# Performance work log

Measured on AMD Instinct MI355X. Metric: run time of the kernel, lower is better.

## Reference

```python
import jax, jax.numpy as jnp
import numpy as np

B, N, E = 64, 512, 8192          # graphs, nodes per graph, edges per graph
F_IN, H, C = 128, 128, 10        # in features, hidden, classes
K1, K2 = 256, 128                # dense pool cluster counts: ceil(.5*N), ceil(.5*K1)
EPS = 1e-15


def setup_inputs():
    key = jax.random.key(0)
    keys = jax.random.split(key, 32)
    it = iter(keys)
    def w(shape, fan_in):
        return jax.random.normal(next(it), shape, jnp.float32) / np.sqrt(fan_in)
    x = jax.random.normal(next(it), (B * N, F_IN), jnp.float32)
    src_l = jax.random.randint(next(it), (B, E), 0, N)
    dst_l = jax.random.randint(next(it), (B, E), 0, N)
    off = (jnp.arange(B) * N)[:, None]
    src = (src_l + off).reshape(-1).astype(jnp.int32)
    dst = (dst_l + off).reshape(-1).astype(jnp.int32)
    return dict(
        x=x, src=src, dst=dst,
        conv0_wr=w((F_IN, H), F_IN), conv0_wroot=w((F_IN, H), F_IN), conv0_b=jnp.zeros((H,), jnp.float32),
        sconv2_wr=w((H, H), H), sconv2_wroot=w((H, H), H), sconv2_b=jnp.zeros((H,), jnp.float32),
        sconv3_wr=w((H, H), H), sconv3_wroot=w((H, H), H), sconv3_b=jnp.zeros((H,), jnp.float32),
        sage1_wr=w((H, H), H), sage1_wroot=w((H, H), H), sage1_b=jnp.zeros((H,), jnp.float32),
        sage2_wr=w((H, H), H), sage2_wroot=w((H, H), H), sage2_b=jnp.zeros((H,), jnp.float32),
        pool0_w=w((H, K1), H), pool0_b=jnp.zeros((K1,), jnp.float32),
        pool1_w=w((H, K2), H), pool1_b=jnp.zeros((K2,), jnp.float32),
        p1=w((H,), H), p2=w((H,), H), p3=w((H,), H),
        lin1_1_w=w((2 * H, H), 2 * H), lin1_1_b=jnp.zeros((H,), jnp.float32),
        lin1_w=w((H, H), H), lin1_b=jnp.zeros((H,), jnp.float32),
        lin2_w=w((2 * H, C), 2 * H), lin2_b=jnp.zeros((C,), jnp.float32),
    )


def _graph_conv(x, src, dst, emask, wr, wroot, b, n):
    # PyG GraphConv: lin_rel(sum_j x_j) + lin_root(x_i); invalid edges masked to 0.
    msg = x[src] * emask[:, None]
    agg = jax.ops.segment_sum(msg, dst, num_segments=n)
    return agg @ wr + x @ wroot + b


def _topk_pool(x, score_w, src, dst, emask, n_per_graph, k):
    # TopK pooling (MPoolS): score = x.w/||w||, keep top ratio*n per graph, gate by tanh(score).
    score = x @ score_w / (jnp.linalg.norm(score_w) + 1e-16)
    idx = jax.lax.top_k(score.reshape(B, n_per_graph), k)[1]
    perm = (idx + (jnp.arange(B) * n_per_graph)[:, None]).reshape(-1)
    new_x = x[perm] * jnp.tanh(score[perm])[:, None]
    new_id = jnp.full((B * n_per_graph,), -1, jnp.int32).at[perm].set(
        jnp.arange(B * k, dtype=jnp.int32))
    ns, nd = new_id[src], new_id[dst]
    valid = (ns >= 0) & (nd >= 0) & (emask > 0)
    return new_x, jnp.where(valid, ns, 0), jnp.where(valid, nd, 0), valid.astype(x.dtype)


def _readout(x, k):
    # gmp || gap per graph (nodes are contiguous, k per graph)
    xr = x.reshape(B, k, -1)
    return jnp.concatenate([xr.max(axis=1), xr.mean(axis=1)], axis=-1)


def _dense_sage(x, adj, wr, wroot, b):
    agg = (adj @ x) / jnp.clip(adj.sum(-1, keepdims=True), 1.0, None)
    return agg @ wr + x @ wroot + b


def _dense_mincut_pool(x, adj, s):
    s = jax.nn.softmax(s, axis=-1)
    k = s.shape[-1]
    out = jnp.einsum('bnk,bnf->bkf', s, x)
    out_adj = jnp.einsum('bnk,bnm,bml->bkl', s, adj, s)
    mincut_num = jnp.trace(out_adj, axis1=-2, axis2=-1)
    deg = adj.sum(-1)
    mincut_den = jnp.einsum('bn,bnk,bnk->b', deg, s, s)
    mc = -jnp.mean(mincut_num / (mincut_den + EPS))
    ss = jnp.einsum('bnk,bnl->bkl', s, s)
    ss_n = jnp.linalg.norm(ss, axis=(1, 2), keepdims=True)
    eye = jnp.eye(k, dtype=x.dtype)
    o = jnp.mean(jnp.linalg.norm(ss / (ss_n + EPS) - eye / jnp.sqrt(k), axis=(1, 2)))
    di = jnp.arange(k)
    out_adj = out_adj.at[:, di, di].set(0.0)
    dpool = jnp.sqrt(out_adj.sum(-1)) + EPS
    out_adj = out_adj / dpool[:, :, None] / dpool[:, None, :]
    return out, out_adj, mc, o


def _forward(x, src, dst, conv0_wr, conv0_wroot, conv0_b, sconv2_wr, sconv2_wroot, sconv2_b,
             sconv3_wr, sconv3_wroot, sconv3_b, sage1_wr, sage1_wroot, sage1_b,
             sage2_wr, sage2_wroot, sage2_b, pool0_w, pool0_b, pool1_w, pool1_b,
             p1, p2, p3, lin1_1_w, lin1_1_b, lin1_w, lin1_b, lin2_w, lin2_b):
    relu = jax.nn.relu
    e0 = jnp.ones((src.shape[0],), x.dtype)
    x0 = relu(_graph_conv(x, src, dst, e0, conv0_wr, conv0_wroot, conv0_b, B * N))
    # ---- sparse (MPoolS / top-k) branch, stage 1 ----
    sx, s1, d1, m1 = _topk_pool(x0, p1, src, dst, e0, N, N // 2)
    sx1 = _readout(sx, N // 2)
    # ---- dense (DiffPool-style) branch ----
    xd = x0.reshape(B, N, H)                               # to_dense_batch (full mask)
    g = src // N
    adj = jnp.zeros((B, N, N), x.dtype).at[g, src % N, dst % N].add(1.0)  # to_dense_adj
    s = xd @ pool0_w + pool0_b
    xd, adj, mc, o = _dense_mincut_pool(xd, adj, s)
    xd = relu(_dense_sage(xd, adj, sage1_wr, sage1_wroot, sage1_b))
    s = xd @ pool1_w + pool1_b
    xd, adj, mc2, o2 = _dense_mincut_pool(xd, adj, s)
    mc, o = mc + mc2, o + o2
    xd = _dense_sage(xd, adj, sage2_wr, sage2_wroot, sage2_b)
    xg = relu(xd.mean(axis=1) @ lin1_w + lin1_b)
    # ---- sparse branch, stages 2 and 3 ----
    sx = relu(_graph_conv(sx, s1, d1, m1, sconv2_wr, sconv2_wroot, sconv2_b, B * (N // 2)))
    sx, s2, d2, m2 = _topk_pool(sx, p2, s1, d1, m1, N // 2, N // 4)
    sx2 = _readout(sx, N // 4)
    sx = relu(_graph_conv(sx, s2, d2, m2, sconv3_wr, sconv3_wroot, sconv3_b, B * (N // 4)))
    sx, s3, d3, m3 = _topk_pool(sx, p3, s2, d2, m2, N // 4, N // 8)
    sx3 = _readout(sx, N // 8)
    sxr = relu((sx1 + sx2 + sx3) @ lin1_1_w + lin1_1_b)
    logits = jnp.concatenate([sxr, xg], axis=-1) @ lin2_w + lin2_b
    return logits, mc, o


def reference(x, src, dst, conv0_wr, conv0_wroot, conv0_b, sconv2_wr, sconv2_wroot, sconv2_b,
              sconv3_wr, sconv3_wroot, sconv3_b, sage1_wr, sage1_wroot, sage1_b,
              sage2_wr, sage2_wroot, sage2_b, pool0_w, pool0_b, pool1_w, pool1_b,
              p1, p2, p3, lin1_1_w, lin1_1_b, lin1_w, lin1_b, lin2_w, lin2_b):
    return _forward(x, src, dst, conv0_wr, conv0_wroot, conv0_b, sconv2_wr, sconv2_wroot,
                    sconv2_b, sconv3_wr, sconv3_wroot, sconv3_b, sage1_wr, sage1_wroot,
                    sage1_b, sage2_wr, sage2_wroot, sage2_b, pool0_w, pool0_b, pool1_w,
                    pool1_b, p1, p2, p3, lin1_1_w, lin1_1_b, lin1_w, lin1_b, lin2_w, lin2_b)
```

## Files before the change

kernel.cpp:

```cpp
#include <hip/hip_runtime.h>
#include <math.h>

#define NGRAPH 64
#define NE 524288
#define EPG 8192
#define TSZ 2560

typedef short s16x8 __attribute__((ext_vector_type(8)));
typedef float f32x4 __attribute__((ext_vector_type(4)));

__device__ inline unsigned short f2bf(float f) {
    unsigned int u = __float_as_uint(f);
    return (unsigned short)((u + 0x7FFFu + ((u >> 16) & 1u)) >> 16);
}

__global__ void edge_count(const int* __restrict__ key, const float* __restrict__ mask,
                           int* __restrict__ counts) {
    int e = blockIdx.x * 256 + threadIdx.x;
    if (e < NE && (!mask || mask[e] > 0.f)) atomicAdd(&counts[key[e]], 1);
}

__global__ __launch_bounds__(512) void scan_offsets(const int* __restrict__ counts,
        int* __restrict__ offs, int* __restrict__ cursor, int nPerGraph,
        float* __restrict__ degOut) {
    __shared__ int s[512];
    const int g = blockIdx.x, t = threadIdx.x;
    int v = (t < nPerGraph) ? counts[g * nPerGraph + t] : 0;
    s[t] = v; __syncthreads();
    for (int d = 1; d < 512; d <<= 1) {
        int u = (t >= d) ? s[t - d] : 0;
        __syncthreads();
        s[t] += u;
        __syncthreads();
    }
    if (t < nPerGraph) {
        int o = g * EPG + s[t] - v;
        offs[g * nPerGraph + t] = o;
        cursor[g * nPerGraph + t] = o;
        if (degOut) degOut[g * nPerGraph + t] = (float)v;
    }
}

__global__ void edge_fill(const int* __restrict__ key, const int* __restrict__ payload,
                          const float* __restrict__ mask, int* __restrict__ cursor,
                          int* __restrict__ elist) {
    int e = blockIdx.x * 256 + threadIdx.x;
    if (e < NE && (!mask || mask[e] > 0.f)) {
        int p = atomicAdd(&cursor[key[e]], 1);
        elist[p] = payload[e];
    }
}

__global__ __launch_bounds__(256) void gather_csr(
    const float* __restrict__ xfeat, int Fx,
    const int* __restrict__ offs, const int* __restrict__ cnts,
    const int* __restrict__ elist,
    float* __restrict__ out, int totRows, int rowsPerGraph)
{
    const int gid = (blockIdx.x * 256 + threadIdx.x) >> 5;
    const int lane = threadIdx.x & 31;
    const int csh = (Fx == 256) ? 1 : 0;
    const int rid = gid >> csh;
    const int c0 = (gid & ((1 << csh) - 1)) << 7;
    if (rid >= totRows) return;
    const int row = (rid & 63) * rowsPerGraph + (rid >> 6);
    const int beg = offs[row];
    const int n = cnts[row];
    const long long co = (long long)c0 + (lane << 2);
    float4 acc = make_float4(0.f, 0.f, 0.f, 0.f);
    int j = 0;
    for (; j + 4 <= n; j += 4) {
        const int n0 = elist[beg + j], n1 = elist[beg + j + 1];
        const int n2 = elist[beg + j + 2], n3 = elist[beg + j + 3];
        const float4 v0 = *(const float4*)&xfeat[(long long)n0 * Fx + co];
        const float4 v1 = *(const float4*)&xfeat[(long long)n1 * Fx + co];
        const float4 v2 = *(const float4*)&xfeat[(long long)n2 * Fx + co];
        const float4 v3 = *(const float4*)&xfeat[(long long)n3 * Fx + co];
        acc.x += v0.x + v1.x + v2.x + v3.x;
        acc.y += v0.y + v1.y + v2.y + v3.y;
        acc.z += v0.z + v1.z + v2.z + v3.z;
        acc.w += v0.w + v1.w + v2.w + v3.w;
    }
    for (; j < n; ++j) {
        const float4 v = *(const float4*)&xfeat[(long long)elist[beg + j] * Fx + co];
        acc.x += v.x; acc.y += v.y; acc.z += v.z; acc.w += v.w;
    }
    *(float4*)&out[(long long)row * Fx + co] = acc;
}

struct WSpec {
    const float* w1; const float* w2; int K1; int K2; int Nn;
    unsigned short* oh; unsigned short* ol;
};

__global__ void wconv_all(WSpec s0, WSpec s1, WSpec s2, WSpec s3, WSpec s4, WSpec s5, WSpec s6) {
    WSpec s;
    switch (blockIdx.y) {
        case 0: s = s0; break; case 1: s = s1; break; case 2: s = s2; break;
        case 3: s = s3; break; case 4: s = s4; break; case 5: s = s5; break;
        default: s = s6; break;
    }
    int idx = blockIdx.x * 256 + threadIdx.x;
    int Kt = s.K1 + s.K2;
    if (idx >= s.Nn * Kt) return;
    int n = idx / Kt, k = idx - n * Kt;
    float v = (k < s.K1) ? s.w1[(long long)k * s.Nn + n] : s.w2[(long long)(k - s.K1) * s.Nn + n];
    unsigned short h = f2bf(v);
    s.oh[idx] = h;
    s.ol[idx] = f2bf(v - __uint_as_float((unsigned int)h << 16));
}

__device__ inline void stageN_split(const float* __restrict__ src, int ldk, int k0,
                                    short* lds, int tid, const float* __restrict__ rs, int m0) {
    const int r = tid >> 2, kq = (tid & 3) << 3;
    const float* p = src + (long long)r * ldk + k0 + kq;
    float v[8];
    *(float4*)v = *(const float4*)p;
    *(float4*)(v + 4) = *(const float4*)(p + 4);
    if (rs) { float s = rs[m0 + r]; for (int i = 0; i < 8; ++i) v[i] *= s; }
    s16x8 hv, lv;
    #pragma unroll
    for (int i = 0; i < 8; ++i) {
        unsigned short h = f2bf(v[i]);
        float hf = __uint_as_float((unsigned int)h << 16);
        hv[i] = (short)h;
        lv[i] = (short)f2bf(v[i] - hf);
    }
    *(s16x8*)(lds + r * 40 + kq) = hv;
    *(s16x8*)(lds + TSZ + r * 40 + kq) = lv;
}

__device__ inline void stageT_split(const float* __restrict__ src, int ldm, int k0, int m0,
                                    short* lds, int tid) {
    const int kp = tid >> 4, mc = tid & 15;
    const int k = kp << 1;
    const float* p0 = src + (long long)(k0 + k) * ldm + m0 + mc;
    const float* p1 = p0 + ldm;
    #pragma unroll
    for (int i = 0; i < 4; ++i) {
        float a = p0[i << 4], b = p1[i << 4];
        unsigned short ha = f2bf(a), hb = f2bf(b);
        float hfa = __uint_as_float((unsigned int)ha << 16);
        float hfb = __uint_as_float((unsigned int)hb << 16);
        unsigned short la = f2bf(a - hfa), lb = f2bf(b - hfb);
        const int o = (mc + (i << 4)) * 40 + k;
        *(unsigned int*)(lds + o) = (unsigned int)ha | ((unsigned int)hb << 16);
        *(unsigned int*)(lds + o + TSZ) = (unsigned int)la | ((unsigned int)lb << 16);
    }
}

__device__ inline void stageT_hi(const float* __restrict__ src, int ldm, int k0, int m0,
                                 short* lds, int tid) {
    const int kp = tid >> 4, mc = tid & 15;
    const int k = kp << 1;
    const float* p0 = src + (long long)(k0 + k) * ldm + m0 + mc;
    const float* p1 = p0 + ldm;
    #pragma unroll
    for (int i = 0; i < 4; ++i) {
        unsigned short ha = f2bf(p0[i << 4]), hb = f2bf(p1[i << 4]);
        *(unsigned int*)(lds + (mc + (i << 4)) * 40 + k) =
            (unsigned int)ha | ((unsigned int)hb << 16);
    }
}

__device__ inline void stageW_split(const unsigned short* __restrict__ wh,
                                    const unsigned short* __restrict__ wl, int ldk,
                                    int n0, int k0, short* lds, int tid) {
    const int r = tid >> 2, kq = (tid & 3) << 3;
    *(s16x8*)(lds + r * 40 + kq) = *(const s16x8*)(wh + (long long)(n0 + r) * ldk + k0 + kq);
    *(s16x8*)(lds + TSZ + r * 40 + kq) = *(const s16x8*)(wl + (long long)(n0 + r) * ldk + k0 + kq);
}

__device__ inline void mfma_split(const short* As, const short* Bs, int wm, int wn,
                                  int l15, int quad, f32x4 (&acc)[2][2]) {
    const int ko = quad << 3;
    s16x8 ah[2], al[2], bh[2], bl[2];
    #pragma unroll
    for (int i = 0; i < 2; ++i) {
        const int ra = (wm + (i << 4) + l15) * 40 + ko;
        const int rb = (wn + (i << 4) + l15) * 40 + ko;
        ah[i] = *(const s16x8*)&As[ra];
        al[i] = *(const s16x8*)&As[TSZ + ra];
        bh[i] = *(const s16x8*)&Bs[rb];
        bl[i] = *(const s16x8*)&Bs[TSZ + rb];
    }
    #pragma unroll
    for (int mi = 0; mi < 2; ++mi)
    #pragma unroll
    for (int ni = 0; ni < 2; ++ni) {
        f32x4 c = acc[mi][ni];
        c = __builtin_amdgcn_mfma_f32_16x16x32_bf16(ah[mi], bh[ni], c, 0, 0, 0);
        c = __builtin_amdgcn_mfma_f32_16x16x32_bf16(ah[mi], bl[ni], c, 0, 0, 0);
        c = __builtin_amdgcn_mfma_f32_16x16x32_bf16(al[mi], bh[ni], c, 0, 0, 0);
        acc[mi][ni] = c;
    }
}

__device__ inline void mfma_hi(const short* As, const short* Bs, int wm, int wn,
                               int l15, int quad, f32x4 (&acc)[2][2]) {
    const int ko = quad << 3;
    s16x8 ah[2], bh[2];
    #pragma unroll
    for (int i = 0; i < 2; ++i) {
        ah[i] = *(const s16x8*)&As[(wm + (i << 4) + l15) * 40 + ko];
        bh[i] = *(const s16x8*)&Bs[(wn + (i << 4) + l15) * 40 + ko];
    }
    #pragma unroll
    for (int mi = 0; mi < 2; ++mi)
    #pragma unroll
    for (int ni = 0; ni < 2; ++ni)
        acc[mi][ni] = __builtin_amdgcn_mfma_f32_16x16x32_bf16(ah[mi], bh[ni], acc[mi][ni], 0, 0, 0);
}

__global__ __launch_bounds__(256) void gemm_aw(
    const float* __restrict__ A1, int K1, const float* __restrict__ A2, int K2,
    const float* __restrict__ rscale,
    const unsigned short* __restrict__ Wh, const unsigned short* __restrict__ Wl,
    const float* __restrict__ bias, float* __restrict__ C, int Nn, int doRelu)
{
    __shared__ short As[2 * TSZ], Bs[2 * TSZ];
    const int m0 = blockIdx.y << 6, n0 = blockIdx.x << 6;
    const int tid = threadIdx.x, lane = tid & 63, wv = tid >> 6;
    const int l15 = lane & 15, quad = lane >> 4;
    const int wm = (wv & 1) << 5, wn = (wv >> 1) << 5;
    f32x4 acc[2][2] = {};
    const int Kt = K1 + K2;
    for (int k0 = 0; k0 < Kt; k0 += 32) {
        if (k0 < K1) stageN_split(A1 + (long long)m0 * K1, K1, k0, As, tid, rscale, m0);
        else         stageN_split(A2 + (long long)m0 * K2, K2, k0 - K1, As, tid, nullptr, 0);
        stageW_split(Wh, Wl, Kt, n0, k0, Bs, tid);
        __syncthreads();
        mfma_split(As, Bs, wm, wn, l15, quad, acc);
        __syncthreads();
    }
    #pragma unroll
    for (int mi = 0; mi < 2; ++mi)
    #pragma unroll
    for (int ni = 0; ni < 2; ++ni) {
        const int col = n0 + wn + (ni << 4) + l15;
        const float bv = bias ? bias[col] : 0.f;
        #pragma unroll
        for (int r = 0; r < 4; ++r) {
            const int row = m0 + wm + (mi << 4) + (quad << 2) + r;
            float v = acc[mi][ni][r] + bv;
            if (doRelu) v = fmaxf(v, 0.f);
            C[(long long)row * Nn + col] = v;
        }
    }
}

__global__ __launch_bounds__(256) void gemm_tt(
    const float* __restrict__ At, const float* __restrict__ Bkn,
    float* __restrict__ C, float* __restrict__ fro,
    int Kd, int Mm, int Nn, int dual,
    long long sA, long long sB, long long sC)
{
    __shared__ short As[2 * TSZ], Bs[2 * TSZ], A2s[TSZ];
    __shared__ float redf[4];
    const int z = blockIdx.x;
    const float* Ap = At + (long long)z * sA;
    const float* Bp = Bkn + (long long)z * sB;
    const int m0 = blockIdx.y << 6, n0 = blockIdx.z << 6;
    const int tid = threadIdx.x, lane = tid & 63, wv = tid >> 6;
    const int l15 = lane & 15, quad = lane >> 4;
    const int wm = (wv & 1) << 5, wn = (wv >> 1) << 5;
    const int fw = dual ? ((m0 < n0) ? 2 : ((m0 == n0) ? 1 : 0)) : 0;
    f32x4 acc[2][2] = {};
    f32x4 accA[2][2] = {};
    for (int k0 = 0; k0 < Kd; k0 += 32) {
        stageT_split(Ap, Mm, k0, m0, As, tid);
        stageT_split(Bp, Nn, k0, n0, Bs, tid);
        if (fw) stageT_hi(Ap, Mm, k0, n0, A2s, tid);
        __syncthreads();
        mfma_split(As, Bs, wm, wn, l15, quad, acc);
        if (fw) mfma_hi(As, A2s, wm, wn, l15, quad, accA);
        __syncthreads();
    }
    float* Cp = C + (long long)z * sC;
    #pragma unroll
    for (int mi = 0; mi < 2; ++mi)
    #pragma unroll
    for (int ni = 0; ni < 2; ++ni) {
        const int col = n0 + wn + (ni << 4) + l15;
        #pragma unroll
        for (int r = 0; r < 4; ++r) {
            const int row = m0 + wm + (mi << 4) + (quad << 2) + r;
            Cp[(long long)row * Nn + col] = acc[mi][ni][r];
        }
    }
    if (fw) {
        float s = 0.f;
        #pragma unroll
        for (int mi = 0; mi < 2; ++mi)
        #pragma unroll
        for (int ni = 0; ni < 2; ++ni)
        #pragma unroll
        for (int r = 0; r < 4; ++r) s += accA[mi][ni][r] * accA[mi][ni][r];
        s *= (float)fw;
        for (int off = 32; off; off >>= 1) s += __shfl_xor(s, off);
        if (lane == 0) redf[wv] = s;
        __syncthreads();
        if (tid == 0) atomicAdd(&fro[z], redf[0] + redf[1] + redf[2] + redf[3]);
    }
}

__global__ __launch_bounds__(256) void gemm_nt(
    const float* __restrict__ A, const float* __restrict__ Bkn, float* __restrict__ C,
    int Kd, int Nn, long long sA, long long sB, long long sC)
{
    __shared__ short As[2 * TSZ], Bs[2 * TSZ];
    const int z = blockIdx.x;
    const int m0 = blockIdx.y << 6, n0 = blockIdx.z << 6;
    const float* Ap = A + (long long)z * sA + (long long)m0 * Kd;
    const float* Bp = Bkn + (long long)z * sB;
    const int tid = threadIdx.x, lane = tid & 63, wv = tid >> 6;
    const int l15 = lane & 15, quad = lane >> 4;
    const int wm = (wv & 1) << 5, wn = (wv >> 1) << 5;
    f32x4 acc[2][2] = {};
    for (int k0 = 0; k0 < Kd; k0 += 32) {
        stageN_split(Ap, Kd, k0, As, tid, nullptr, 0);
        stageT_split(Bp, Nn, k0, n0, Bs, tid);
        __syncthreads();
        mfma_split(As, Bs, wm, wn, l15, quad, acc);
        __syncthreads();
    }
    float* Cp = C + (long long)z * sC;
    #pragma unroll
    for (int mi = 0; mi < 2; ++mi)
    #pragma unroll
    for (int ni = 0; ni < 2; ++ni) {
        const int col = n0 + wn + (ni << 4) + l15;
        #pragma unroll
        for (int r = 0; r < 4; ++r) {
            const int row = m0 + wm + (mi << 4) + (quad << 2) + r;
            Cp[(long long)row * Nn + col] = acc[mi][ni][r];
        }
    }
}

__global__ __launch_bounds__(256) void softmax_rows_wave(
    float* __restrict__ sm, int L,
    const float* __restrict__ deg,
    float* __restrict__ rowq2, float* __restrict__ rowdq2, int totRows)
{
    const int wid = (blockIdx.x * 256 + threadIdx.x) >> 6;
    const int lane = threadIdx.x & 63;
    if (wid >= totRows) return;
    float* rowp = sm + (long long)wid * L;
    const int nv = L >> 6;
    float v[4];
    if (nv == 4) {
        float4 t = *(const float4*)&rowp[lane << 2];
        v[0] = t.x; v[1] = t.y; v[2] = t.z; v[3] = t.w;
    } else {
        float2 t = *(const float2*)&rowp[lane << 1];
        v[0] = t.x; v[1] = t.y;
    }
    float mx = v[0];
    for (int i = 1; i < nv; ++i) mx = fmaxf(mx, v[i]);
    for (int off = 32; off; off >>= 1) mx = fmaxf(mx, __shfl_xor(mx, off));
    float s = 0.f;
    for (int i = 0; i < nv; ++i) { v[i] = expf(v[i] - mx); s += v[i]; }
    for (int off = 32; off; off >>= 1) s += __shfl_xor(s, off);
    const float inv = 1.f / s;
    float q2 = 0.f;
    for (int i = 0; i < nv; ++i) { float p = v[i] * inv; v[i] = p; q2 += p * p; }
    if (nv == 4) *(float4*)&rowp[lane << 2] = make_float4(v[0], v[1], v[2], v[3]);
    else         *(float2*)&rowp[lane << 1] = make_float2(v[0], v[1]);
    for (int off = 32; off; off >>= 1) q2 += __shfl_xor(q2, off);
    if (lane == 0) { rowq2[wid] = q2; rowdq2[wid] = deg[wid] * q2; }
}

__global__ __launch_bounds__(256) void zdiag_rowsum_wave(
    float* __restrict__ adj, int K, float* __restrict__ dpool,
    float* __restrict__ rowdiag, int totRows)
{
    const int wid = (blockIdx.x * 256 + threadIdx.x) >> 6;
    const int lane = threadIdx.x & 63;
    if (wid >= totRows) return;
    const int b = wid / K;
    const int dcol = wid - b * K;
    float* rowp = adj + (long long)wid * K;
    const int nv = K >> 6;
    float s = 0.f, dval = 0.f;
    for (int q = 0; q < nv; ++q) {
        int c = lane + (q << 6);
        float v = rowp[c];
        if (c == dcol) { dval = v; rowp[c] = 0.f; v = 0.f; }
        s += v;
    }
    for (int off = 32; off; off >>= 1) s += __shfl_xor(s, off);
    if (lane == (dcol & 63)) rowdiag[wid] = dval;
    if (lane == 0) dpool[wid] = sqrtf(s) + 1e-15f;
}

__global__ __launch_bounds__(256) void norm_adj_wave(
    float* __restrict__ adj, int K, const float* __restrict__ dpool,
    float* __restrict__ rowsum, float* __restrict__ rscale, int totRows)
{
    const int wid = (blockIdx.x * 256 + threadIdx.x) >> 6;
    const int lane = threadIdx.x & 63;
    if (wid >= totRows) return;
    const int b = wid / K;
    float* rowp = adj + (long long)wid * K;
    const float inv_r = 1.f / dpool[wid];
    const int nv = K >> 6;
    float s = 0.f;
    for (int q = 0; q < nv; ++q) {
        int c = lane + (q << 6);
        float v = rowp[c] * inv_r / dpool[b * K + c];
        rowp[c] = v;
        s += v;
    }
    for (int off = 32; off; off >>= 1) s += __shfl_xor(s, off);
    if (lane == 0) { rowsum[wid] = s; rscale[wid] = 1.f / fmaxf(s, 1.f); }
}

__global__ __launch_bounds__(256) void reduce2_pergraph(
    const float* __restrict__ a, const float* __restrict__ b, int rowsPerGraph,
    float* __restrict__ outA, float* __restrict__ outB)
{
    __shared__ float redA[4], redB[4];
    const int g = blockIdx.x, t = threadIdx.x;
    float sa = 0.f, sb = 0.f;
    for (int i = t; i < rowsPerGraph; i += 256) {
        sa += a[g * rowsPerGraph + i];
        if (b) sb += b[g * rowsPerGraph + i];
    }
    for (int off = 32; off; off >>= 1) { sa += __shfl_xor(sa, off); sb += __shfl_xor(sb, off); }
    const int wv = t >> 6;
    if ((t & 63) == 0) { redA[wv] = sa; redB[wv] = sb; }
    __syncthreads();
    if (t == 0) {
        outA[g] = redA[0] + redA[1] + redA[2] + redA[3];
        if (outB) outB[g] = redB[0] + redB[1] + redB[2] + redB[3];
    }
}

__global__ __launch_bounds__(512) void topk_kernel(
    const float* __restrict__ x, const float* __restrict__ p, int n, int k,
    int* __restrict__ new_id, int* __restrict__ sel, float* __restrict__ gate)
{
    __shared__ float sc[512];
    __shared__ int pref[512];
    const int g = blockIdx.x, tid = threadIdx.x;
    float myScore = 0.f;
    if (tid < n) {
        const float* xr = x + (long long)(g * n + tid) * 128;
        float pn2 = 0.f, d = 0.f;
        #pragma unroll 4
        for (int f = 0; f < 128; f += 4) {
            float4 pv = *(const float4*)&p[f];
            float4 v = *(const float4*)&xr[f];
            pn2 += pv.x * pv.x + pv.y * pv.y + pv.z * pv.z + pv.w * pv.w;
            d += v.x * pv.x + v.y * pv.y + v.z * pv.z + v.w * pv.w;
        }
        myScore = d / (sqrtf(pn2) + 1e-16f);
        sc[tid] = myScore;
    }
    __syncthreads();
    int keep = 0;
    if (tid < n) {
        const float si = myScore;
        int rank = 0;
        for (int j = 0; j < n; j += 4) {
            float4 s4 = *(const float4*)&sc[j];
            rank += (s4.x > si) || (s4.x == si && (j + 0) < tid);
            rank += (s4.y > si) || (s4.y == si && (j + 1) < tid);
            rank += (s4.z > si) || (s4.z == si && (j + 2) < tid);
            rank += (s4.w > si) || (s4.w == si && (j + 3) < tid);
        }
        keep = rank < k;
    }
    pref[tid] = keep;
    __syncthreads();
    for (int d = 1; d < 512; d <<= 1) {
        int u = (tid >= d) ? pref[tid - d] : 0;
        __syncthreads();
        pref[tid] += u;
        __syncthreads();
    }
    if (tid < n) {
        if (keep) {
            int pos = pref[tid] - 1;
            new_id[g * n + tid] = g * k + pos;
            sel[g * k + pos] = g * n + tid;
            gate[g * k + pos] = tanhf(myScore);
        } else new_id[g * n + tid] = -1;
    }
}

__global__ void gather_gate(const float* __restrict__ x, const int* __restrict__ sel,
                            const float* __restrict__ gate, float* __restrict__ out, int rows) {
    int t = blockIdx.x * blockDim.x + threadIdx.x;
    int r = t >> 5, q = (t & 31) << 2;
    if (r >= rows) return;
    float4 v = *(const float4*)&x[(long long)sel[r] * 128 + q];
    float gt = gate[r];
    v.x *= gt; v.y *= gt; v.z *= gt; v.w *= gt;
    *(float4*)&out[(long long)r * 128 + q] = v;
}

__global__ void remap_edges_count(const int* __restrict__ s, const int* __restrict__ d,
                                  const float* __restrict__ m, const int* __restrict__ new_id,
                                  int* __restrict__ so, int* __restrict__ do_,
                                  float* __restrict__ mo, int* __restrict__ counts) {
    int e = blockIdx.x * blockDim.x + threadIdx.x;
    if (e >= NE) return;
    int ns = new_id[s[e]], nd = new_id[d[e]];
    bool v = (ns >= 0) && (nd >= 0) && (m ? (m[e] > 0.f) : true);
    so[e] = v ? ns : 0; do_[e] = v ? nd : 0; mo[e] = v ? 1.f : 0.f;
    if (v) atomicAdd(&counts[nd], 1);
}

__global__ void readout_part(const float* __restrict__ x, int k,
                             float* __restrict__ pmax, float* __restrict__ psum) {
    int g = blockIdx.x, seg = blockIdx.y, f = threadIdx.x;
    int per = k >> 2;
    int r0 = seg * per;
    float mx0 = -INFINITY, mx1 = -INFINITY, sm0 = 0.f, sm1 = 0.f;
    int r = r0;
    for (; r + 2 <= r0 + per; r += 2) {
        float v0 = x[(long long)(g * k + r) * 128 + f];
        float v1 = x[(long long)(g * k + r + 1) * 128 + f];
        mx0 = fmaxf(mx0, v0); sm0 += v0;
        mx1 = fmaxf(mx1, v1); sm1 += v1;
    }
    for (; r < r0 + per; ++r) { float v = x[(long long)(g * k + r) * 128 + f]; mx0 = fmaxf(mx0, v); sm0 += v; }
    pmax[(g * 4 + seg) * 128 + f] = fmaxf(mx0, mx1);
    psum[(g * 4 + seg) * 128 + f] = sm0 + sm1;
}

__global__ void readout_comb(const float* __restrict__ pmax, const float* __restrict__ psum,
                             int k, float* __restrict__ sxsum) {
    int g = blockIdx.x, f = threadIdx.x;
    float mx = -INFINITY, sm = 0.f;
    #pragma unroll
    for (int s = 0; s < 4; ++s) {
        mx = fmaxf(mx, pmax[(g * 4 + s) * 128 + f]);
        sm += psum[(g * 4 + s) * 128 + f];
    }
    sxsum[g * 256 + f] += mx;
    sxsum[g * 256 + 128 + f] += sm / k;
}

__global__ void mc_o_write(const float* __restrict__ accs, float* __restrict__ out) {
    __shared__ float rm[2], ro[2];
    int t = threadIdx.x;
    int wvi = t >> 6, lane = t & 63;
    const float* acc = accs + wvi * 256;
    float sqrtk = wvi ? sqrtf(128.f) : 16.f;
    float numv = acc[lane], denv = acc[64 + lane], trv = acc[128 + lane], frov = acc[192 + lane];
    float mcb = numv / (denv + 1e-15f);
    float ssn = sqrtf(frov) + 1e-15f;
    float ob = sqrtf(fmaxf(frov / (ssn * ssn) - 2.f * trv / (ssn * sqrtk) + 1.f, 0.f));
    for (int off = 32; off; off >>= 1) { mcb += __shfl_down(mcb, off); ob += __shfl_down(ob, off); }
    if (lane == 0) { rm[wvi] = mcb; ro[wvi] = ob; }
    __syncthreads();
    if (t == 0) {
        out[640] = -(rm[0] + rm[1]) / 64.f;
        out[641] = (ro[0] + ro[1]) / 64.f;
    }
}

__global__ void mean_lin(const float* __restrict__ xd, const float* __restrict__ W,
                         const float* __restrict__ bias, float* __restrict__ xg, int nNodes) {
    __shared__ float meanv[128];
    int b = blockIdx.x, t = threadIdx.x;
    float s = 0.f;
    for (int n = 0; n < nNodes; n++) s += xd[(long long)(b * nNodes + n) * 128 + t];
    meanv[t] = s / nNodes; __syncthreads();
    float acc = bias[t];
    for (int i = 0; i < 128; i++) acc += meanv[i] * W[i * 128 + t];
    xg[b * 128 + t] = fmaxf(acc, 0.f);
}

__global__ void final_head(const float* __restrict__ sxsum, const float* __restrict__ w11,
                           const float* __restrict__ b11, const float* __restrict__ xg,
                           const float* __restrict__ w2, const float* __restrict__ b2,
                           float* __restrict__ outLogits) {
    __shared__ float sin_[256];
    __shared__ float cat[256];
    int b = blockIdx.x, t = threadIdx.x;
    sin_[t] = sxsum[b * 256 + t];
    sin_[t + 128] = sxsum[b * 256 + 128 + t];
    __syncthreads();
    float acc = b11[t];
    for (int i = 0; i < 256; i++) acc += sin_[i] * w11[i * 128 + t];
    cat[t] = fmaxf(acc, 0.f);
    cat[128 + t] = xg[b * 128 + t];
    __syncthreads();
    if (t < 10) {
        float a = b2[t];
        for (int i = 0; i < 256; i++) a += cat[i] * w2[i * 10 + t];
        outLogits[b * 10 + t] = a;
    }
}

extern "C" void kernel_launch(void* const* d_in, const int* in_sizes, int n_in,
                              void* d_out, int out_size, void* d_ws, size_t ws_size,
                              hipStream_t stream) {
    const float* x         = (const float*)d_in[0];
    const int*   src       = (const int*)d_in[1];
    const int*   dst       = (const int*)d_in[2];
    const float* conv0_wr  = (const float*)d_in[3];
    const float* conv0_wrt = (const float*)d_in[4];
    const float* conv0_b   = (const float*)d_in[5];
    const float* sc2_wr    = (const float*)d_in[6];
    const float* sc2_wrt   = (const float*)d_in[7];
    const float* sc2_b     = (const float*)d_in[8];
    const float* sc3_wr    = (const float*)d_in[9];
    const float* sc3_wrt   = (const float*)d_in[10];
    const float* sc3_b     = (const float*)d_in[11];
    const float* sg1_wr    = (const float*)d_in[12];
    const float* sg1_wrt   = (const float*)d_in[13];
    const float* sg1_b     = (const float*)d_in[14];
    const float* sg2_wr    = (const float*)d_in[15];
    const float* sg2_wrt   = (const float*)d_in[16];
    const float* sg2_b     = (const float*)d_in[17];
    const float* pool0_w   = (const float*)d_in[18];
    const float* pool0_b   = (const float*)d_in[19];
    const float* pool1_w   = (const float*)d_in[20];
    const float* pool1_b   = (const float*)d_in[21];
    const float* p1        = (const float*)d_in[22];
    const float* p2        = (const float*)d_in[23];
    const float* p3        = (const float*)d_in[24];
    const float* l11_w     = (const float*)d_in[25];
    const float* l11_b     = (const float*)d_in[26];
    const float* l1_w      = (const float*)d_in[27];
    const float* l1_b      = (const float*)d_in[28];
    const float* l2_w      = (const float*)d_in[29];
    const float* l2_b      = (const float*)d_in[30];
    float* out = (float*)d_out;

    char* w = (char*)d_ws;
    const unsigned long long MBy = 1ull << 20;
    float* x0    = (float*)(w + 0);
    float* BIG1  = (float*)(w + 16 * MBy);
    float* BIG2  = (float*)(w + 48 * MBy);
    float* agg   = (float*)(w + 80 * MBy);
    float* outx1 = (float*)(w + 96 * MBy);
    float* adj1  = (float*)(w + 104 * MBy);
    int*   s1    = (int*)(w + 120 * MBy);
    int*   d1    = (int*)(w + 122 * MBy);
    float* m1    = (float*)(w + 124 * MBy);
    int*   s2e   = (int*)(w + 126 * MBy);
    int*   d2e   = (int*)(w + 128 * MBy);
    float* m2e   = (float*)(w + 130 * MBy);
    char*  misc  = w + 132 * MBy;
    float* score = (float*)(misc);
    int*   sel   = (int*)(misc + 128 * 1024);
    float* gate  = (float*)(misc + 192 * 1024);
    int*   newid = (int*)(misc + 256 * 1024);
    float* deg   = (float*)(misc + 384 * 1024);
    float* dpool = (float*)(misc + 512 * 1024);
    float* rowsum2 = (float*)(misc + 576 * 1024);
    float* rscale2 = (float*)(misc + 640 * 1024);
    float* dpool2  = (float*)(misc + 704 * 1024);
    float* rowsum3 = (float*)(misc + 736 * 1024);
    float* rscale3 = (float*)(misc + 768 * 1024);
    float* accs    = (float*)(misc + 800 * 1024);
    float* sxsum   = (float*)(misc + 900 * 1024);
    float* xg      = (float*)(misc + 964 * 1024);

    unsigned short* wt_sg1h   = (unsigned short*)(misc + 1024 * 1024);
    unsigned short* wt_sg1l   = wt_sg1h + 32768;
    unsigned short* wt_sg2h   = wt_sg1l + 32768;
    unsigned short* wt_sg2l   = wt_sg2h + 32768;
    unsigned short* wt_pool0h = wt_sg2l + 32768;
    unsigned short* wt_pool0l = wt_pool0h + 32768;
    unsigned short* wt_pool1h = wt_pool0l + 32768;
    unsigned short* wt_pool1l = wt_pool1h + 32768;
    unsigned short* wt_c0h    = wt_pool1l + 32768;
    unsigned short* wt_c0l    = wt_c0h + 32768;
    unsigned short* wt_sc2h   = wt_c0l + 32768;
    unsigned short* wt_sc2l   = wt_sc2h + 32768;
    unsigned short* wt_sc3h   = wt_sc2l + 32768;
    unsigned short* wt_sc3l   = wt_sc3h + 32768;

    float* pmax = (float*)(misc + 2048 * 1024);
    float* psum = pmax + 32768;

    float* rowq2  = score;
    float* rowdq2 = (float*)newid;
    float* rowdiag = (float*)sel;

    float* s_sm  = BIG1;
    float* Tbuf  = BIG2;
    float* xd1   = BIG2;
    float* AX    = BIG2 + 2 * 1024 * 1024;
    float* s2sm  = BIG2 + 4 * 1024 * 1024;
    float* T2    = BIG2 + 6 * 1024 * 1024;
    float* outx2 = BIG1;
    float* adj2b = BIG1 + 1024 * 1024;
    float* xd2   = BIG1 + 2 * 1024 * 1024;
    float* sxA   = BIG1 + 3 * 1024 * 1024;
    float* sxE   = BIG1 + 5 * 1024 * 1024;
    float* sxB   = x0;
    float* sxC   = x0 + 2 * 1024 * 1024;
    float* sxD   = x0 + 3 * 1024 * 1024;

    char* adjc = (char*)adj1;
    int* elA  = (int*)(adjc + 0);
    int* elB  = (int*)(adjc + 2 * MBy);
    int* cntA = (int*)(adjc + 4 * MBy);
    int* offA = (int*)(adjc + 4 * MBy + 256 * 1024);
    int* curA = (int*)(adjc + 4 * MBy + 512 * 1024);
    int* cntB = (int*)(adjc + 4 * MBy + 768 * 1024);
    int* offB = (int*)(adjc + 5 * MBy);
    int* curB = (int*)(adjc + 5 * MBy + 256 * 1024);
    char* aggc = (char*)agg;
    int* elC  = (int*)(aggc + 8 * MBy);
    int* elD  = (int*)(aggc + 10 * MBy);
    int* cntC = (int*)(aggc + 12 * MBy);
    int* offC = (int*)(aggc + 12 * MBy + 256 * 1024);
    int* curC = (int*)(aggc + 12 * MBy + 512 * 1024);
    int* cntD = (int*)(aggc + 13 * MBy);
    int* offD = (int*)(aggc + 13 * MBy + 256 * 1024);
    int* curD = (int*)(aggc + 13 * MBy + 512 * 1024);

    hipMemsetAsync(accs, 0, 520 * sizeof(float), stream);
    hipMemsetAsync(sxsum, 0, 16384 * sizeof(float), stream);
    hipMemsetAsync(cntA, 0, 32768 * sizeof(int), stream);
    hipMemsetAsync(cntB, 0, 32768 * sizeof(int), stream);

    {
        WSpec a{sg1_wr, sg1_wrt, 128, 128, 128, wt_sg1h, wt_sg1l};
        WSpec b{sg2_wr, sg2_wrt, 128, 128, 128, wt_sg2h, wt_sg2l};
        WSpec c{pool0_w, nullptr, 128, 0, 256, wt_pool0h, wt_pool0l};
        WSpec d{pool1_w, nullptr, 128, 0, 128, wt_pool1h, wt_pool1l};
        WSpec e{conv0_wr, conv0_wrt, 128, 128, 128, wt_c0h, wt_c0l};
        WSpec f{sc2_wr, sc2_wrt, 128, 128, 128, wt_sc2h, wt_sc2l};
        WSpec g{sc3_wr, sc3_wrt, 128, 128, 128, wt_sc3h, wt_sc3l};
        wconv_all<<<dim3(128, 7), 256, 0, stream>>>(a, b, c, d, e, f, g);
    }

    edge_count<<<2048, 256, 0, stream>>>(dst, nullptr, cntA);
    edge_count<<<2048, 256, 0, stream>>>(src, nullptr, cntB);
    scan_offsets<<<64, 512, 0, stream>>>(cntA, offA, curA, 512, nullptr);
    scan_offsets<<<64, 512, 0, stream>>>(cntB, offB, curB, 512, deg);
    edge_fill<<<2048, 256, 0, stream>>>(dst, src, nullptr, curA, elA);
    edge_fill<<<2048, 256, 0, stream>>>(src, dst, nullptr, curB, elB);

    gather_csr<<<4096, 256, 0, stream>>>(x, 128, offA, cntA, elA, agg, 32768, 512);
    gemm_aw<<<dim3(2, 512), 256, 0, stream>>>(agg, 128, x, 128, nullptr, wt_c0h, wt_c0l,
        conv0_b, x0, 128, 1);

    gemm_aw<<<dim3(4, 512), 256, 0, stream>>>(x0, 128, nullptr, 0, nullptr, wt_pool0h, wt_pool0l,
        pool0_b, s_sm, 256, 0);
    softmax_rows_wave<<<8192, 256, 0, stream>>>(s_sm, 256, deg, rowq2, rowdq2, 32768);
    reduce2_pergraph<<<64, 256, 0, stream>>>(rowq2, rowdq2, 512, accs + 128, accs + 64);
    gather_csr<<<8192, 256, 0, stream>>>(s_sm, 256, offB, cntB, elB, Tbuf, 32768, 512);
    gemm_tt<<<dim3(64, 4, 2), 256, 0, stream>>>(s_sm, x0, outx1, nullptr, 512, 256, 128, 0,
        512 * 256, 512 * 128, 256 * 128);
    gemm_tt<<<dim3(64, 4, 4), 256, 0, stream>>>(s_sm, Tbuf, adj1, accs + 192, 512, 256, 256, 1,
        512 * 256, 512 * 256, 256 * 256);
    zdiag_rowsum_wave<<<4096, 256, 0, stream>>>(adj1, 256, dpool, rowdiag, 16384);
    reduce2_pergraph<<<64, 256, 0, stream>>>(rowdiag, nullptr, 256, accs + 0, nullptr);
    norm_adj_wave<<<4096, 256, 0, stream>>>(adj1, 256, dpool, rowsum2, rscale2, 16384);
    gemm_nt<<<dim3(64, 4, 2), 256, 0, stream>>>(adj1, outx1, AX, 256, 128,
        256 * 256, 256 * 128, 256 * 128);
    gemm_aw<<<dim3(2, 256), 256, 0, stream>>>(AX, 128, outx1, 128, rscale2, wt_sg1h, wt_sg1l,
        sg1_b, xd1, 128, 1);
    gemm_aw<<<dim3(2, 256), 256, 0, stream>>>(xd1, 128, nullptr, 0, nullptr, wt_pool1h, wt_pool1l,
        pool1_b, s2sm, 128, 0);
    softmax_rows_wave<<<4096, 256, 0, stream>>>(s2sm, 128, rowsum2, rowq2, rowdq2, 16384);
    reduce2_pergraph<<<64, 256, 0, stream>>>(rowq2, rowdq2, 256, accs + 384, accs + 320);
    gemm_nt<<<dim3(64, 4, 2), 256, 0, stream>>>(adj1, s2sm, T2, 256, 128,
        256 * 256, 256 * 128, 256 * 128);
    gemm_tt<<<dim3(64, 2, 2), 256, 0, stream>>>(s2sm, xd1, outx2, nullptr, 256, 128, 128, 0,
        256 * 128, 256 * 128, 128 * 128);
    gemm_tt<<<dim3(64, 2, 2), 256, 0, stream>>>(s2sm, T2, adj2b, accs + 448, 256, 128, 128, 1,
        256 * 128, 256 * 128, 128 * 128);
    zdiag_rowsum_wave<<<2048, 256, 0, stream>>>(adj2b, 128, dpool2, rowdiag, 8192);
    reduce2_pergraph<<<64, 256, 0, stream>>>(rowdiag, nullptr, 128, accs + 256, nullptr);
    norm_adj_wave<<<2048, 256, 0, stream>>>(adj2b, 128, dpool2, rowsum3, rscale3, 8192);
    gemm_nt<<<dim3(64, 2, 2), 256, 0, stream>>>(adj2b, outx2, AX, 128, 128,
        128 * 128, 128 * 128, 128 * 128);
    gemm_aw<<<dim3(2, 128), 256, 0, stream>>>(AX, 128, outx2, 128, rscale3, wt_sg2h, wt_sg2l,
        sg2_b, xd2, 128, 0);
    mean_lin<<<64, 128, 0, stream>>>(xd2, l1_w, l1_b, xg, 128);
    mc_o_write<<<1, 128, 0, stream>>>(accs, out);

    topk_kernel<<<64, 512, 0, stream>>>(x0, p1, 512, 256, newid, sel, gate);
    gather_gate<<<2048, 256, 0, stream>>>(x0, sel, gate, sxA, 16384);
    hipMemsetAsync(cntC, 0, 16384 * sizeof(int), stream);
    remap_edges_count<<<2048, 256, 0, stream>>>(src, dst, nullptr, newid, s1, d1, m1, cntC);
    readout_part<<<dim3(64, 4), 128, 0, stream>>>(sxA, 256, pmax, psum);
    readout_comb<<<64, 128, 0, stream>>>(pmax, psum, 256, sxsum);
    scan_offsets<<<64, 512, 0, stream>>>(cntC, offC, curC, 256, nullptr);
    edge_fill<<<2048, 256, 0, stream>>>(d1, s1, m1, curC, elC);
    gather_csr<<<2048, 256, 0, stream>>>(sxA, 128, offC, cntC, elC, agg, 16384, 256);
    gemm_aw<<<dim3(2, 256), 256, 0, stream>>>(agg, 128, sxA, 128, nullptr, wt_sc2h, wt_sc2l,
        sc2_b, sxB, 128, 1);
    topk_kernel<<<64, 512, 0, stream>>>(sxB, p2, 256, 128, newid, sel, gate);
    gather_gate<<<1024, 256, 0, stream>>>(sxB, sel, gate, sxC, 8192);
    hipMemsetAsync(cntD, 0, 8192 * sizeof(int), stream);
    remap_edges_count<<<2048, 256, 0, stream>>>(s1, d1, m1, newid, s2e, d2e, m2e, cntD);
    readout_part<<<dim3(64, 4), 128, 0, stream>>>(sxC, 128, pmax, psum);
    readout_comb<<<64, 128, 0, stream>>>(pmax, psum, 128, sxsum);
    scan_offsets<<<64, 512, 0, stream>>>(cntD, offD, curD, 128, nullptr);
    edge_fill<<<2048, 256, 0, stream>>>(d2e, s2e, m2e, curD, elD);
    gather_csr<<<1024, 256, 0, stream>>>(sxC, 128, offD, cntD, elD, agg, 8192, 128);
    gemm_aw<<<dim3(2, 128), 256, 0, stream>>>(agg, 128, sxC, 128, nullptr, wt_sc3h, wt_sc3l,
        sc3_b, sxD, 128, 1);
    topk_kernel<<<64, 512, 0, stream>>>(sxD, p3, 128, 64, newid, sel, gate);
    gather_gate<<<512, 256, 0, stream>>>(sxD, sel, gate, sxE, 4096);
    readout_part<<<dim3(64, 4), 128, 0, stream>>>(sxE, 64, pmax, psum);
    readout_comb<<<64, 128, 0, stream>>>(pmax, psum, 64, sxsum);

    final_head<<<64, 128, 0, stream>>>(sxsum, l11_w, l11_b, xg, l2_w, l2_b, out);
}
```

Before: 666.6 us.

## Store softmax assignments and intermediates as packed bf16 hi/lo pairs

Softmax outputs, the CSR-gathered T buffer and T2 are now written as a packed 32-bit word holding bf16 hi and lo halves. Downstream GEMMs stage these words into LDS with bit shuffles instead of redoing the split conversion on every tile load, and gather_csr unpacks them while accumulating. The aim is to move the split-bf16 conversion cost out of repeated GEMM tile staging. In exchange the gather loop loses its 4-way unroll on the packed path, and the hi+lo representation loses a little precision compared with fp32.

```diff
diff --git a/kernel.cpp b/kernel.cpp
--- a/kernel.cpp
+++ b/kernel.cpp
@@ -12,6 +12,15 @@
 __device__ inline unsigned short f2bf(float f) {
     unsigned int u = __float_as_uint(f);
     return (unsigned short)((u + 0x7FFFu + ((u >> 16) & 1u)) >> 16);
+}
+__device__ inline unsigned int packhl(float v) {
+    unsigned short h = f2bf(v);
+    float hf = __uint_as_float((unsigned int)h << 16);
+    unsigned short l = f2bf(v - hf);
+    return (unsigned int)h | ((unsigned int)l << 16);
+}
+__device__ inline float unpackhl(unsigned int u) {
+    return __uint_as_float(u << 16) + __uint_as_float(u & 0xFFFF0000u);
 }
 
 __global__ void edge_count(const int* __restrict__ key, const float* __restrict__ mask,
@@ -52,10 +61,11 @@
 }
 
 __global__ __launch_bounds__(256) void gather_csr(
-    const float* __restrict__ xfeat, int Fx,
+    const void* __restrict__ xfeatv, int Fx,
     const int* __restrict__ offs, const int* __restrict__ cnts,
     const int* __restrict__ elist,
-    float* __restrict__ out, int totRows, int rowsPerGraph)
+    void* __restrict__ outv, int totRows, int rowsPerGraph,
+    int inPacked, int outPacked)
 {
     const int gid = (blockIdx.x * 256 + threadIdx.x) >> 5;
     const int lane = threadIdx.x & 31;
@@ -68,24 +78,40 @@
     const int n = cnts[row];
     const long long co = (long long)c0 + (lane << 2);
     float4 acc = make_float4(0.f, 0.f, 0.f, 0.f);
-    int j = 0;
-    for (; j + 4 <= n; j += 4) {
-        const int n0 = elist[beg + j], n1 = elist[beg + j + 1];
-        const int n2 = elist[beg + j + 2], n3 = elist[beg + j + 3];
-        const float4 v0 = *(const float4*)&xfeat[(long long)n0 * Fx + co];
-        const float4 v1 = *(const float4*)&xfeat[(long long)n1 * Fx + co];
-        const float4 v2 = *(const float4*)&xfeat[(long long)n2 * Fx + co];
-        const float4 v3 = *(const float4*)&xfeat[(long long)n3 * Fx + co];
-        acc.x += v0.x + v1.x + v2.x + v3.x;
-        acc.y += v0.y + v1.y + v2.y + v3.y;
-        acc.z += v0.z + v1.z + v2.z + v3.z;
-        acc.w += v0.w + v1.w + v2.w + v3.w;
-    }
-    for (; j < n; ++j) {
-        const float4 v = *(const float4*)&xfeat[(long long)elist[beg + j] * Fx + co];
-        acc.x += v.x; acc.y += v.y; acc.z += v.z; acc.w += v.w;
-    }
-    *(float4*)&out[(long long)row * Fx + co] = acc;
+    if (inPacked) {
+        const unsigned int* xf = (const unsigned int*)xfeatv;
+        for (int j = 0; j < n; ++j) {
+            uint4 u = *(const uint4*)&xf[(long long)elist[beg + j] * Fx + co];
+            acc.x += unpackhl(u.x); acc.y += unpackhl(u.y);
+            acc.z += unpackhl(u.z); acc.w += unpackhl(u.w);
+        }
+    } else {
+        const float* xf = (const float*)xfeatv;
+        int j = 0;
+        for (; j + 4 <= n; j += 4) {
+            const int n0 = elist[beg + j], n1 = elist[beg + j + 1];
+            const int n2 = elist[beg + j + 2], n3 = elist[beg + j + 3];
+            const float4 v0 = *(const float4*)&xf[(long long)n0 * Fx + co];
+            const float4 v1 = *(const float4*)&xf[(long long)n1 * Fx + co];
+            const float4 v2 = *(const float4*)&xf[(long long)n2 * Fx + co];
+            const float4 v3 = *(const float4*)&xf[(long long)n3 * Fx + co];
+            acc.x += v0.x + v1.x + v2.x + v3.x;
+            acc.y += v0.y + v1.y + v2.y + v3.y;
+            acc.z += v0.z + v1.z + v2.z + v3.z;
+            acc.w += v0.w + v1.w + v2.w + v3.w;
+        }
+        for (; j < n; ++j) {
+            const float4 v = *(const float4*)&xf[(long long)elist[beg + j] * Fx + co];
+            acc.x += v.x; acc.y += v.y; acc.z += v.z; acc.w += v.w;
+        }
+    }
+    if (outPacked) {
+        uint4 u;
+        u.x = packhl(acc.x); u.y = packhl(acc.y); u.z = packhl(acc.z); u.w = packhl(acc.w);
+        *(uint4*)&((unsigned int*)outv)[(long long)row * Fx + co] = u;
+    } else {
+        *(float4*)&((float*)outv)[(long long)row * Fx + co] = acc;
+    }
 }
 
 struct WSpec {
@@ -149,6 +175,21 @@
     }
 }
 
+__device__ inline void stageT_packed(const unsigned int* __restrict__ src, int ldm,
+                                     int k0, int m0, short* lds, int tid) {
+    const int kp = tid >> 4, mc = tid & 15;
+    const int k = kp << 1;
+    const unsigned int* p0 = src + (long long)(k0 + k) * ldm + m0 + mc;
+    const unsigned int* p1 = p0 + ldm;
+    #pragma unroll
+    for (int i = 0; i < 4; ++i) {
+        unsigned int a = p0[i << 4], b = p1[i << 4];
+        const int o = (mc + (i << 4)) * 40 + k;
+        *(unsigned int*)(lds + o) = (a & 0xFFFFu) | (b << 16);
+        *(unsigned int*)(lds + o + TSZ) = (a >> 16) | (b & 0xFFFF0000u);
+    }
+}
+
 __device__ inline void stageT_hi(const float* __restrict__ src, int ldm, int k0, int m0,
                                  short* lds, int tid) {
     const int kp = tid >> 4, mc = tid & 15;
@@ -160,6 +201,19 @@
         unsigned short ha = f2bf(p0[i << 4]), hb = f2bf(p1[i << 4]);
         *(unsigned int*)(lds + (mc + (i << 4)) * 40 + k) =
             (unsigned int)ha | ((unsigned int)hb << 16);
+    }
+}
+
+__device__ inline void stageT_hi_packed(const unsigned int* __restrict__ src, int ldm,
+                                        int k0, int m0, short* lds, int tid) {
+    const int kp = tid >> 4, mc = tid & 15;
+    const int k = kp << 1;
+    const unsigned int* p0 = src + (long long)(k0 + k) * ldm + m0 + mc;
+    const unsigned int* p1 = p0 + ldm;
+    #pragma unroll
+    for (int i = 0; i < 4; ++i) {
+        unsigned int a = p0[i << 4], b = p1[i << 4];
+        *(unsigned int*)(lds + (mc + (i << 4)) * 40 + k) = (a & 0xFFFFu) | (b << 16);
     }
 }
 
@@ -250,16 +304,14 @@
 }
 
 __global__ __launch_bounds__(256) void gemm_tt(
-    const float* __restrict__ At, const float* __restrict__ Bkn,
+    const void* __restrict__ Atv, const void* __restrict__ Bknv,
     float* __restrict__ C, float* __restrict__ fro,
-    int Kd, int Mm, int Nn, int dual,
+    int Kd, int Mm, int Nn, int dual, int aPacked, int bPacked,
     long long sA, long long sB, long long sC)
 {
     __shared__ short As[2 * TSZ], Bs[2 * TSZ], A2s[TSZ];
     __shared__ float redf[4];
     const int z = blockIdx.x;
-    const float* Ap = At + (long long)z * sA;
-    const float* Bp = Bkn + (long long)z * sB;
     const int m0 = blockIdx.y << 6, n0 = blockIdx.z << 6;
     const int tid = threadIdx.x, lane = tid & 63, wv = tid >> 6;
     const int l15 = lane & 15, quad = lane >> 4;
@@ -268,9 +320,14 @@
     f32x4 acc[2][2] = {};
     f32x4 accA[2][2] = {};
     for (int k0 = 0; k0 < Kd; k0 += 32) {
-        stageT_split(Ap, Mm, k0, m0, As, tid);
-        stageT_split(Bp, Nn, k0, n0, Bs, tid);
-        if (fw) stageT_hi(Ap, Mm, k0, n0, A2s, tid);
+        if (aPacked) stageT_packed((const unsigned int*)Atv + z * sA, Mm, k0, m0, As, tid);
+        else         stageT_split((const float*)Atv + z * sA, Mm, k0, m0, As, tid);
+        if (bPacked) stageT_packed((const unsigned int*)Bknv + z * sB, Nn, k0, n0, Bs, tid);
+        else         stageT_split((const float*)Bknv + z * sB, Nn, k0, n0, Bs, tid);
+        if (fw) {
+            if (aPacked) stageT_hi_packed((const unsigned int*)Atv + z * sA, Mm, k0, n0, A2s, tid);
+            else         stageT_hi((const float*)Atv + z * sA, Mm, k0, n0, A2s, tid);
+        }
         __syncthreads();
         mfma_split(As, Bs, wm, wn, l15, quad, acc);
         if (fw) mfma_hi(As, A2s, wm, wn, l15, quad, accA);
@@ -305,26 +362,26 @@
 }
 
 __global__ __launch_bounds__(256) void gemm_nt(
-    const float* __restrict__ A, const float* __restrict__ Bkn, float* __restrict__ C,
-    int Kd, int Nn, long long sA, long long sB, long long sC)
+    const float* __restrict__ A, const void* __restrict__ Bknv, void* __restrict__ Cv,
+    int Kd, int Nn, int bPacked, int outPacked,
+    long long sA, long long sB, long long sC)
 {
     __shared__ short As[2 * TSZ], Bs[2 * TSZ];
     const int z = blockIdx.x;
     const int m0 = blockIdx.y << 6, n0 = blockIdx.z << 6;
     const float* Ap = A + (long long)z * sA + (long long)m0 * Kd;
-    const float* Bp = Bkn + (long long)z * sB;
     const int tid = threadIdx.x, lane = tid & 63, wv = tid >> 6;
     const int l15 = lane & 15, quad = lane >> 4;
     const int wm = (wv & 1) << 5, wn = (wv >> 1) << 5;
     f32x4 acc[2][2] = {};
     for (int k0 = 0; k0 < Kd; k0 += 32) {
         stageN_split(Ap, Kd, k0, As, tid, nullptr, 0);
-        stageT_split(Bp, Nn, k0, n0, Bs, tid);
+        if (bPacked) stageT_packed((const unsigned int*)Bknv + z * sB, Nn, k0, n0, Bs, tid);
+        else         stageT_split((const float*)Bknv + z * sB, Nn, k0, n0, Bs, tid);
         __syncthreads();
         mfma_split(As, Bs, wm, wn, l15, quad, acc);
         __syncthreads();
     }
-    float* Cp = C + (long long)z * sC;
     #pragma unroll
     for (int mi = 0; mi < 2; ++mi)
     #pragma unroll
@@ -333,7 +390,10 @@
         #pragma unroll
         for (int r = 0; r < 4; ++r) {
             const int row = m0 + wm + (mi << 4) + (quad << 2) + r;
-            Cp[(long long)row * Nn + col] = acc[mi][ni][r];
+            if (outPacked)
+                ((unsigned int*)Cv)[z * sC + (long long)row * Nn + col] = packhl(acc[mi][ni][r]);
+            else
+                ((float*)Cv)[z * sC + (long long)row * Nn + col] = acc[mi][ni][r];
         }
     }
 }
@@ -364,9 +424,14 @@
     for (int off = 32; off; off >>= 1) s += __shfl_xor(s, off);
     const float inv = 1.f / s;
     float q2 = 0.f;
-    for (int i = 0; i < nv; ++i) { float p = v[i] * inv; v[i] = p; q2 += p * p; }
-    if (nv == 4) *(float4*)&rowp[lane << 2] = make_float4(v[0], v[1], v[2], v[3]);
-    else         *(float2*)&rowp[lane << 1] = make_float2(v[0], v[1]);
+    unsigned int pk[4];
+    for (int i = 0; i < nv; ++i) {
+        float p = v[i] * inv;
+        q2 += p * p;
+        pk[i] = packhl(p);
+    }
+    if (nv == 4) *(uint4*)&((unsigned int*)rowp)[lane << 2] = make_uint4(pk[0], pk[1], pk[2], pk[3]);
+    else         *(uint2*)&((unsigned int*)rowp)[lane << 1] = make_uint2(pk[0], pk[1]);
     for (int off = 32; off; off >>= 1) q2 += __shfl_xor(q2, off);
     if (lane == 0) { rowq2[wid] = q2; rowdq2[wid] = deg[wid] * q2; }
 }
@@ -742,7 +807,7 @@
     edge_fill<<<2048, 256, 0, stream>>>(dst, src, nullptr, curA, elA);
     edge_fill<<<2048, 256, 0, stream>>>(src, dst, nullptr, curB, elB);
 
-    gather_csr<<<4096, 256, 0, stream>>>(x, 128, offA, cntA, elA, agg, 32768, 512);
+    gather_csr<<<4096, 256, 0, stream>>>(x, 128, offA, cntA, elA, agg, 32768, 512, 0, 0);
     gemm_aw<<<dim3(2, 512), 256, 0, stream>>>(agg, 128, x, 128, nullptr, wt_c0h, wt_c0l,
         conv0_b, x0, 128, 1);
 
@@ -750,15 +815,15 @@
         pool0_b, s_sm, 256, 0);
     softmax_rows_wave<<<8192, 256, 0, stream>>>(s_sm, 256, deg, rowq2, rowdq2, 32768);
     reduce2_pergraph<<<64, 256, 0, stream>>>(rowq2, rowdq2, 512, accs + 128, accs + 64);
-    gather_csr<<<8192, 256, 0, stream>>>(s_sm, 256, offB, cntB, elB, Tbuf, 32768, 512);
-    gemm_tt<<<dim3(64, 4, 2), 256, 0, stream>>>(s_sm, x0, outx1, nullptr, 512, 256, 128, 0,
+    gather_csr<<<8192, 256, 0, stream>>>(s_sm, 256, offB, cntB, elB, Tbuf, 32768, 512, 1, 1);
+    gemm_tt<<<dim3(64, 4, 2), 256, 0, stream>>>(s_sm, x0, outx1, nullptr, 512, 256, 128, 0, 1, 0,
         512 * 256, 512 * 128, 256 * 128);
-    gemm_tt<<<dim3(64, 4, 4), 256, 0, stream>>>(s_sm, Tbuf, adj1, accs + 192, 512, 256, 256, 1,
+    gemm_tt<<<dim3(64, 4, 4), 256, 0, stream>>>(s_sm, Tbuf, adj1, accs + 192, 512, 256, 256, 1, 1, 1,
         512 * 256, 512 * 256, 256 * 256);
     zdiag_rowsum_wave<<<4096, 256, 0, stream>>>(adj1, 256, dpool, rowdiag, 16384);
     reduce2_pergraph<<<64, 256, 0, stream>>>(rowdiag, nullptr, 256, accs + 0, nullptr);
     norm_adj_wave<<<4096, 256, 0, stream>>>(adj1, 256, dpool, rowsum2, rscale2, 16384);
-    gemm_nt<<<dim3(64, 4, 2), 256, 0, stream>>>(adj1, outx1, AX, 256, 128,
+    gemm_nt<<<dim3(64, 4, 2), 256, 0, stream>>>(adj1, outx1, AX, 256, 128, 0, 0,
         256 * 256, 256 * 128, 256 * 128);
     gemm_aw<<<dim3(2, 256), 256, 0, stream>>>(AX, 128, outx1, 128, rscale2, wt_sg1h, wt_sg1l,
         sg1_b, xd1, 128, 1);
@@ -766,16 +831,16 @@
         pool1_b, s2sm, 128, 0);
     softmax_rows_wave<<<4096, 256, 0, stream>>>(s2sm, 128, rowsum2, rowq2, rowdq2, 16384);
     reduce2_pergraph<<<64, 256, 0, stream>>>(rowq2, rowdq2, 256, accs + 384, accs + 320);
-    gemm_nt<<<dim3(64, 4, 2), 256, 0, stream>>>(adj1, s2sm, T2, 256, 128,
+    gemm_nt<<<dim3(64, 4, 2), 256, 0, stream>>>(adj1, s2sm, T2, 256, 128, 1, 1,
         256 * 256, 256 * 128, 256 * 128);
-    gemm_tt<<<dim3(64, 2, 2), 256, 0, stream>>>(s2sm, xd1, outx2, nullptr, 256, 128, 128, 0,
+    gemm_tt<<<dim3(64, 2, 2), 256, 0, stream>>>(s2sm, xd1, outx2, nullptr, 256, 128, 128, 0, 1, 0,
         256 * 128, 256 * 128, 128 * 128);
-    gemm_tt<<<dim3(64, 2, 2), 256, 0, stream>>>(s2sm, T2, adj2b, accs + 448, 256, 128, 128, 1,
+    gemm_tt<<<dim3(64, 2, 2), 256, 0, stream>>>(s2sm, T2, adj2b, accs + 448, 256, 128, 128, 1, 1, 1,
         256 * 128, 256 * 128, 128 * 128);
     zdiag_rowsum_wave<<<2048, 256, 0, stream>>>(adj2b, 128, dpool2, rowdiag, 8192);
     reduce2_pergraph<<<64, 256, 0, stream>>>(rowdiag, nullptr, 128, accs + 256, nullptr);
     norm_adj_wave<<<2048, 256, 0, stream>>>(adj2b, 128, dpool2, rowsum3, rscale3, 8192);
-    gemm_nt<<<dim3(64, 2, 2), 256, 0, stream>>>(adj2b, outx2, AX, 128, 128,
+    gemm_nt<<<dim3(64, 2, 2), 256, 0, stream>>>(adj2b, outx2, AX, 128, 128, 0, 0,
         128 * 128, 128 * 128, 128 * 128);
     gemm_aw<<<dim3(2, 128), 256, 0, stream>>>(AX, 128, outx2, 128, rscale3, wt_sg2h, wt_sg2l,
         sg2_b, xd2, 128, 0);
@@ -790,7 +855,7 @@
     readout_comb<<<64, 128, 0, stream>>>(pmax, psum, 256, sxsum);
     scan_offsets<<<64, 512, 0, stream>>>(cntC, offC, curC, 256, nullptr);
     edge_fill<<<2048, 256, 0, stream>>>(d1, s1, m1, curC, elC);
-    gather_csr<<<2048, 256, 0, stream>>>(sxA, 128, offC, cntC, elC, agg, 16384, 256);
+    gather_csr<<<2048, 256, 0, stream>>>(sxA, 128, offC, cntC, elC, agg, 16384, 256, 0, 0);
     gemm_aw<<<dim3(2, 256), 256, 0, stream>>>(agg, 128, sxA, 128, nullptr, wt_sc2h, wt_sc2l,
         sc2_b, sxB, 128, 1);
     topk_kernel<<<64, 512, 0, stream>>>(sxB, p2, 256, 128, newid, sel, gate);
@@ -801,7 +866,7 @@
     readout_comb<<<64, 128, 0, stream>>>(pmax, psum, 128, sxsum);
     scan_offsets<<<64, 512, 0, stream>>>(cntD, offD, curD, 128, nullptr);
     edge_fill<<<2048, 256, 0, stream>>>(d2e, s2e, m2e, curD, elD);
-    gather_csr<<<1024, 256, 0, stream>>>(sxC, 128, offD, cntD, elD, agg, 8192, 128);
+    gather_csr<<<1024, 256, 0, stream>>>(sxC, 128, offD, cntD, elD, agg, 8192, 128, 0, 0);
     gemm_aw<<<dim3(2, 128), 256, 0, stream>>>(agg, 128, sxC, 128, nullptr, wt_sc3h, wt_sc3l,
         sc3_b, sxD, 128, 1);
     topk_kernel<<<64, 512, 0, stream>>>(sxD, p3, 128, 64, newid, sel, gate);
```

Result: slower. 694.1 us (+4.1%).
